# Kernel optimization log

Hardware: AMD Instinct MI355X
Metric: run time of the kernel (lower is better)

Reference implementation:

```python
import jax, jax.numpy as jnp
import numpy as np

K = 3; PAD = 1; CIN = 64; COUT = 64; B = 4; H = 128; W = 128


def setup_inputs() -> dict:
    key = jax.random.key(0)
    k1, k2, k3 = jax.random.split(key, 3)
    x = jax.random.normal(k1, (B, CIN, H, W), dtype=jnp.float32)
    # offset-predicting conv: [2*K*K, Cin, K, K]; small init -> sub-pixel offsets
    w_off = jax.random.normal(k2, (2 * K * K, CIN, K, K), dtype=jnp.float32) * 0.01
    b_off = jnp.zeros((2 * K * K,), dtype=jnp.float32)
    # deformable conv weight (bias=False): [Cout, Cin, K, K]
    w_def = jax.random.normal(k3, (COUT, CIN, K, K), dtype=jnp.float32) * 0.05
    return {"x": x, "w_off": w_off, "b_off": b_off, "w_def": w_def}


def _deform_conv(x, w_off, b_off, w_def):
    Bb, Cin, Hh, Ww = x.shape
    KK = K * K
    # 1) predict offsets with a regular 3x3 conv (stride 1, pad 1)
    off = jax.lax.conv_general_dilated(
        x, w_off, window_strides=(1, 1), padding=[(PAD, PAD), (PAD, PAD)],
        dimension_numbers=("NCHW", "OIHW", "NCHW"))
    off = off + b_off[None, :, None, None]          # [B, 2*KK, H, W]
    off = off.reshape(Bb, KK, 2, Hh, Ww)            # torchvision layout: (dy, dx) per tap
    dy, dx = off[:, :, 0], off[:, :, 1]             # [B, KK, H, W]

    # 2) sampling coordinates: p = p0 + p_k + offset
    ky = (jnp.arange(KK) // K).astype(x.dtype)
    kx = (jnp.arange(KK) % K).astype(x.dtype)
    hh = jnp.arange(Hh, dtype=x.dtype)
    ww = jnp.arange(Ww, dtype=x.dtype)
    py = hh[None, None, :, None] - PAD + ky[None, :, None, None] + dy   # [B,KK,H,W]
    px = ww[None, None, None, :] - PAD + kx[None, :, None, None] + dx

    # 3) bilinear sampling with zero padding outside the image
    y0f = jnp.floor(py); x0f = jnp.floor(px)
    fy = py - y0f; fx = px - x0f
    y0 = y0f.astype(jnp.int32); x0 = x0f.astype(jnp.int32)
    x_flat = x.reshape(Bb, Cin, Hh * Ww)

    def gather(yi, xi):
        valid = (yi >= 0) & (yi < Hh) & (xi >= 0) & (xi < Ww)
        idx = jnp.clip(yi, 0, Hh - 1) * Ww + jnp.clip(xi, 0, Ww - 1)     # [B,KK,H,W]
        g = jax.vmap(lambda xf, ix: xf[:, ix.reshape(-1)])(x_flat, idx)  # [B,Cin,KK*H*W]
        return g.reshape(Bb, Cin, KK, Hh, Ww) * valid[:, None].astype(x.dtype)

    sampled = (gather(y0, x0)         * ((1 - fy) * (1 - fx))[:, None]
             + gather(y0, x0 + 1)     * ((1 - fy) * fx)[:, None]
             + gather(y0 + 1, x0)     * (fy * (1 - fx))[:, None]
             + gather(y0 + 1, x0 + 1) * (fy * fx)[:, None])               # [B,Cin,KK,H,W]

    # 4) convolution accumulation over (Cin, kernel taps)
    return jnp.einsum('bckhw,ock->bohw', sampled, w_def.reshape(COUT, Cin, KK))


def reference(x, w_off, b_off, w_def):
    return _deform_conv(x, w_off, b_off, w_def)
```

## Files before the change

kernel.cpp:

```cpp
#include <hip/hip_runtime.h>
#include <hip/hip_fp16.h>

#define Bn   4
#define CINc 64
#define COUTc 64
#define Hn   128
#define Wn   128
#define HW   (Hn * Wn)
#define KKc  9
#define NOFF 18

typedef short bf16x8 __attribute__((ext_vector_type(8)));
typedef float f32x4  __attribute__((ext_vector_type(4)));
typedef float f32x2  __attribute__((ext_vector_type(2)));

__device__ inline unsigned short f2bf(float f) {
    unsigned int u = __float_as_uint(f);
    return (unsigned short)((u + 0x7fffu + ((u >> 16) & 1u)) >> 16);
}

__device__ inline void dma16(const void* g, void* l) {
#if __has_builtin(__builtin_amdgcn_global_load_lds)
    __builtin_amdgcn_global_load_lds(
        (__attribute__((address_space(1))) void*)(g),
        (__attribute__((address_space(3))) void*)(l), 16, 0, 0);
#else
    *(uint4*)l = *(const uint4*)g;
#endif
}

__global__ __launch_bounds__(256) void prep_all(
        const float* __restrict__ x, unsigned short* __restrict__ xt,
        const float* __restrict__ w_off, const float* __restrict__ w_def,
        unsigned short* __restrict__ wkb_sw, unsigned short* __restrict__ wob_sw) {
    int gb = blockIdx.x;
    int t  = threadIdx.x;
    if (gb < 1024) {
        __shared__ float s[64][65];
        int half = gb & 1;
        int h    = (gb >> 1) & 127;
        int b    = gb >> 8;
        int w0   = half * 64;

        const float* xb = x + (size_t)b * CINc * HW + (size_t)h * Wn + w0;
        int c0 = t >> 4, wq = (t & 15) * 4;
        #pragma unroll
        for (int i = 0; i < 4; ++i) {
            int c = c0 + i * 16;
            float4 v = *(const float4*)(xb + (size_t)c * HW + wq);
            s[c][wq]     = v.x;
            s[c][wq + 1] = v.y;
            s[c][wq + 2] = v.z;
            s[c][wq + 3] = v.w;
        }
        __syncthreads();

        int cpair = t & 31, pxg = t >> 5;
        unsigned* xtp = (unsigned*)xt;
        #pragma unroll
        for (int i = 0; i < 8; ++i) {
            int px = pxg * 8 + i;
            float v0 = s[cpair * 2][px], v1 = s[cpair * 2 + 1][px];
            unsigned d = (unsigned)f2bf(v0) | ((unsigned)f2bf(v1) << 16);
            xtp[(((size_t)(b * Hn + h) * Wn) + w0 + px) * 32 + cpair] = d;
        }
        return;
    }
    int idx = (gb - 1024) * 256 + t;
    if (idx < 36864) {
        int j = idx & 7, l = (idx >> 3) & 63, s = idx >> 9;
        int k = s >> 3, kc = (s >> 2) & 1, ot = s & 3;
        int l15 = l & 15, quad = l >> 4;
        int o = ot * 16 + l15, c = kc * 32 + quad * 8 + j;
        wkb_sw[idx] = f2bf(w_def[((size_t)o * 64 + c) * 9 + k]);
    }
    int i2 = idx - 36864;
    if (i2 >= 0 && i2 < 18432) {
        int j = i2 & 7, l = (i2 >> 3) & 63, s = i2 >> 9;
        int tt = s >> 2, kc = (s >> 1) & 1, mt = s & 1;
        int l15 = l & 15, quad = l >> 4;
        int m = mt * 16 + l15, c = kc * 32 + quad * 8 + j;
        unsigned short v = 0;
        if (m < NOFF) v = f2bf(w_off[((size_t)m * 64 + c) * 9 + tt]);
        wob_sw[i2] = v;
    }
}


#define BFBUILD(C, kc, BF, W0, W1, W2, W3)                                   \
    do {                                                                     \
        const unsigned* t0 = (const unsigned*)&(C)[(kc) * 4 + 0];            \
        const unsigned* t1 = (const unsigned*)&(C)[(kc) * 4 + 1];            \
        const unsigned* b0 = (const unsigned*)&(C)[(kc) * 4 + 2];            \
        const unsigned* b1 = (const unsigned*)&(C)[(kc) * 4 + 3];            \
        _Pragma("unroll")                                                    \
        for (int jd = 0; jd < 4; ++jd) {                                     \
            f32x2 t0p = {__uint_as_float(t0[jd] << 16),                      \
                         __uint_as_float(t0[jd] & 0xFFFF0000u)};             \
            f32x2 t1p = {__uint_as_float(t1[jd] << 16),                      \
                         __uint_as_float(t1[jd] & 0xFFFF0000u)};             \
            f32x2 b0p = {__uint_as_float(b0[jd] << 16),                      \
                         __uint_as_float(b0[jd] & 0xFFFF0000u)};             \
            f32x2 b1p = {__uint_as_float(b1[jd] << 16),                      \
                         __uint_as_float(b1[jd] & 0xFFFF0000u)};             \
            f32x2 vv = t0p * (W0) + t1p * (W1) + b0p * (W2) + b1p * (W3);    \
            unsigned pk;                                                     \
            asm("v_cvt_pk_bf16_f32 %0, %1, %2"                               \
                : "=v"(pk) : "v"(vv.x), "v"(vv.y));                          \
            (BF).u[jd] = pk;                                                 \
        }                                                                    \
    } while (0)

#define TAP(k)                                                               \
    do {                                                                     \
        const uint4* C = R[(k) & 1];                                         \
        union { unsigned u; __half2 hv; } c01, c23;                          \
        c01.u = pw01[(k)]; c23.u = pw23[(k)];                                \
        float W0 = __low2float(c01.hv), W1 = __high2float(c01.hv);           \
        float W2 = __low2float(c23.hv), W3 = __high2float(c23.hv);           \
        union { bf16x8 v; unsigned u[4]; } bfa, bfb;                         \
        BFBUILD(C, 0, bfa, W0, W1, W2, W3);                                  \
        BFBUILD(C, 1, bfb, W0, W1, W2, W3);                                  \
        _Pragma("unroll")                                                    \
        for (int ot = 0; ot < 4; ++ot) {                                     \
            bf16x8 af0 = s_wv[(((k) * 2 + 0) * 4 + ot) * 64 + lane];         \
            acc[ot] = __builtin_amdgcn_mfma_f32_16x16x32_bf16(               \
                af0, bfa.v, acc[ot], 0, 0, 0);                               \
            bf16x8 af1 = s_wv[(((k) * 2 + 1) * 4 + ot) * 64 + lane];         \
            acc[ot] = __builtin_amdgcn_mfma_f32_16x16x32_bf16(               \
                af1, bfb.v, acc[ot], 0, 0, 0);                               \
        }                                                                    \
    } while (0)

#define FETCH_G(kk, st)                                              \
    do {                                                             \
        unsigned ad_ = ad[kk];                                       \
        unsigned xc_ = ad_ >> 16;                                    \
        unsigned at_ = (((ad_ & 255u) << 7) + xc_) << 6;             \
        unsigned ab_ = ((((ad_ >> 8) & 255u) << 7) + xc_) << 6;      \
        R[st][0] = *(const uint4*)(xtb + at_ + co0);                 \
        R[st][1] = *(const uint4*)(xtb + at_ + 64 + co0);            \
        R[st][2] = *(const uint4*)(xtb + ab_ + co0);                 \
        R[st][3] = *(const uint4*)(xtb + ab_ + 64 + co0);            \
        R[st][4] = *(const uint4*)(xtb + at_ + co1);                 \
        R[st][5] = *(const uint4*)(xtb + at_ + 64 + co1);            \
        R[st][6] = *(const uint4*)(xtb + ab_ + co1);                 \
        R[st][7] = *(const uint4*)(xtb + ab_ + 64 + co1);            \
    } while (0)

#define FETCH_L(kk, st)                                              \
    do {                                                             \
        unsigned ad_ = ad[kk];                                       \
        int xc_ = (int)(ad_ >> 16);                                  \
        int r0_ = (int)(ad_ & 255u) - h + 2;                         \
        int r1_ = (int)((ad_ >> 8) & 255u) - h + 2;                  \
        int b00 = (r0_ * 128 + xc_) * 128;                           \
        int b10 = (r1_ * 128 + xc_) * 128;                           \
        int j0  = (quad ^ (xc_ & 7)) << 4;                           \
        int j1  = (quad ^ ((xc_ + 1) & 7)) << 4;                     \
        int j0b = ((4 + quad) ^ (xc_ & 7)) << 4;                     \
        int j1b = ((4 + quad) ^ ((xc_ + 1) & 7)) << 4;               \
        R[st][0] = *(const uint4*)(s_mem + b00 + j0);                \
        R[st][1] = *(const uint4*)(s_mem + b00 + 128 + j1);          \
        R[st][2] = *(const uint4*)(s_mem + b10 + j0);                \
        R[st][3] = *(const uint4*)(s_mem + b10 + 128 + j1);          \
        R[st][4] = *(const uint4*)(s_mem + b00 + j0b);               \
        R[st][5] = *(const uint4*)(s_mem + b00 + 128 + j1b);         \
        R[st][6] = *(const uint4*)(s_mem + b10 + j0b);               \
        R[st][7] = *(const uint4*)(s_mem + b10 + 128 + j1b);         \
    } while (0)

__global__ __launch_bounds__(512, 2) void fused_deform_v20(
        const unsigned short* __restrict__ xt,
        const unsigned short* __restrict__ wob_sw,
        const unsigned short* __restrict__ wkb_sw,
        const float* __restrict__ b_off, float* __restrict__ out) {
    extern __shared__ char s_mem[];
    bf16x8* s_wv = (bf16x8*)(s_mem + 81920);

    int gid  = blockIdx.x;
    int xcd  = gid & 7;
    int j    = gid >> 3;
    int hh   = j & 15;
    int b    = j >> 4;
    int h    = xcd * 16 + hh;
    int tid  = threadIdx.x;
    int lane = tid & 63;
    int wave = __builtin_amdgcn_readfirstlane(tid >> 6);
    int l15  = lane & 15;
    int quad = lane >> 4;
    int p    = wave * 16 + l15;

    const unsigned short* xtb = xt + (size_t)b * HW * 64;

    int xl = lane >> 3;
    int sl = lane & 7;
    #pragma unroll
    for (int i = 0; i < 10; ++i) {
        int slot = i * 8 + wave;
        int r  = slot >> 4;
        int g  = slot & 15;
        int y  = min(max(h - 2 + r, 0), Hn - 1);
        int xx = g * 8 + xl;
        int jj = sl ^ (xx & 7);
        dma16(xtb + ((size_t)y * Wn + xx) * 64 + jj * 8,
              s_mem + (size_t)r * 16384 + (size_t)g * 1024);
    }
    #pragma unroll
    for (int i = 0; i < 5; ++i) {
        int seg = i * 8 + wave;
        if (seg < 36)
            dma16((const uint4*)wob_sw + seg * 64 + lane,
                  s_mem + 81920 + (size_t)seg * 1024);
    }
    __syncthreads();

    f32x4 oa0 = (f32x4){0.f, 0.f, 0.f, 0.f};
    f32x4 oa1 = (f32x4){0.f, 0.f, 0.f, 0.f};
    #pragma unroll
    for (int t9 = 0; t9 < 9; ++t9) {
        int ty = t9 / 3, tx = t9 % 3;
        int y  = h - 1 + ty;
        int xg = p - 1 + tx;
        bool v = (y >= 0) && (y < Hn) && (xg >= 0) && (xg < Wn);
        unsigned m = v ? 0xFFFFFFFFu : 0u;
        int yc = min(max(y, 0), Hn - 1);
        int xc = min(max(xg, 0), Wn - 1);
        int r  = yc - h + 2;
        int base = (r * 128 + xc) * 128;
        uint4 L0 = *(const uint4*)(s_mem + base + ((quad ^ (xc & 7)) << 4));
        uint4 L1 = *(const uint4*)(s_mem + base + (((4 + quad) ^ (xc & 7)) << 4));
        #pragma unroll
        for (int kc = 0; kc < 2; ++kc) {
            union { bf16x8 v; uint4 u; } bf;
            bf.u = kc ? L1 : L0;
            bf.u.x &= m; bf.u.y &= m; bf.u.z &= m; bf.u.w &= m;
            bf16x8 a0 = s_wv[((t9 * 2 + kc) * 2 + 0) * 64 + lane];
            bf16x8 a1 = s_wv[((t9 * 2 + kc) * 2 + 1) * 64 + lane];
            oa0 = __builtin_amdgcn_mfma_f32_16x16x32_bf16(a0, bf.v, oa0, 0, 0, 0);
            oa1 = __builtin_amdgcn_mfma_f32_16x16x32_bf16(a1, bf.v, oa1, 0, 0, 0);
        }
    }

    unsigned my_ad[3]  = {0, 0, 0};
    unsigned my_w01[3] = {0, 0, 0};
    unsigned my_w23[3] = {0, 0, 0};
    auto phase1 = [&](int k, float dy, float dx, int slot) {
        float py  = (float)(h - 1 + k / 3) + dy;
        float pxf = (float)(p - 1 + k % 3) + dx;
        float y0f = floorf(py), x0f = floorf(pxf);
        float fy = py - y0f, fx = pxf - x0f;
        int y0 = (int)y0f, x0 = (int)x0f;
        bool vy0 = (y0 >= 0) & (y0 < Hn);
        bool vy1 = (y0 + 1 >= 0) & (y0 + 1 < Hn);
        bool vx0 = (x0 >= 0) & (x0 < Wn);
        bool vx1 = (x0 + 1 >= 0) & (x0 + 1 < Wn);
        float wy0 = vy0 ? 1.f - fy : 0.f;
        float wy1 = vy1 ? fy : 0.f;
        float wx0 = vx0 ? 1.f - fx : 0.f;
        float wx1 = vx1 ? fx : 0.f;
        int xc = min(max(x0, 0), Wn - 2);
        bool sel0 = (min(max(x0, 0), Wn - 1) != xc);
        bool sel1 = ((min(max(x0 + 1, 0), Wn - 1) - xc) == 1);
        float Wa = (sel0 ? 0.f : wx0) + (sel1 ? 0.f : wx1);
        float Wb = (sel0 ? wx0 : 0.f) + (sel1 ? wx1 : 0.f);
        int yc0 = min(max(y0, 0), Hn - 1), yc1 = min(max(y0 + 1, 0), Hn - 1);
        union { __half2 hv; unsigned u; } c01, c23;
        c01.hv = __floats2half2_rn(wy0 * Wa, wy0 * Wb);
        c23.hv = __floats2half2_rn(wy1 * Wa, wy1 * Wb);
        my_ad[slot]  = (unsigned)yc0 | ((unsigned)yc1 << 8) | ((unsigned)xc << 16);
        my_w01[slot] = c01.u;
        my_w23[slot] = c23.u;
    };
    int kb = quad * 2;
    phase1(kb,     oa0[0] + b_off[4 * quad],     oa0[1] + b_off[4 * quad + 1], 0);
    phase1(kb + 1, oa0[2] + b_off[4 * quad + 2], oa0[3] + b_off[4 * quad + 3], 1);
    if (quad == 0)
        phase1(8, oa1[0] + b_off[16], oa1[1] + b_off[17], 2);
    __syncthreads();

    #pragma unroll
    for (int i = 0; i < 9; ++i) {
        int seg = i * 8 + wave;
        dma16((const uint4*)wkb_sw + (size_t)seg * 64 + lane,
              s_mem + 81920 + (size_t)seg * 1024);
    }

    unsigned ad[KKc], pw01[KKc], pw23[KKc];
    #pragma unroll
    for (int k = 0; k < KKc; ++k) {
        int src  = (k < 8) ? ((k >> 1) * 16 + l15) : l15;
        int slot = (k < 8) ? (k & 1) : 2;
        ad[k]   = (unsigned)__shfl((int)my_ad[slot],  src, 64);
        pw01[k] = (unsigned)__shfl((int)my_w01[slot], src, 64);
        pw23[k] = (unsigned)__shfl((int)my_w23[slot], src, 64);
    }
    __syncthreads();

    bool oow = false;
    #pragma unroll
    for (int k = 0; k < KKc; ++k) {
        int r0 = (int)(ad[k] & 255u) - h + 2;
        int r1 = (int)((ad[k] >> 8) & 255u) - h + 2;
        oow |= ((unsigned)r0 > 4u) | ((unsigned)r1 > 4u);
    }
    bool use_global = __any(oow);

    f32x4 acc[4];
    #pragma unroll
    for (int ot = 0; ot < 4; ++ot) acc[ot] = (f32x4){0.f, 0.f, 0.f, 0.f};

    uint4 R[2][8];
    int co0 = quad * 8, co1 = 32 + quad * 8;

    if (__builtin_expect(use_global, 0)) {
        FETCH_G(0, 0);
        FETCH_G(1, 1); TAP(0);
        FETCH_G(2, 0); TAP(1);
        FETCH_G(3, 1); TAP(2);
        FETCH_G(4, 0); TAP(3);
        FETCH_G(5, 1); TAP(4);
        FETCH_G(6, 0); TAP(5);
        FETCH_G(7, 1); TAP(6);
        FETCH_G(8, 0); TAP(7);
        TAP(8);
    } else {
        FETCH_L(0, 0);
        FETCH_L(1, 1); TAP(0);
        FETCH_L(2, 0); TAP(1);
        FETCH_L(3, 1); TAP(2);
        FETCH_L(4, 0); TAP(3);
        FETCH_L(5, 1); TAP(4);
        FETCH_L(6, 0); TAP(5);
        FETCH_L(7, 1); TAP(6);
        FETCH_L(8, 0); TAP(7);
        TAP(8);
    }

    #pragma unroll
    for (int ot = 0; ot < 4; ++ot)
        #pragma unroll
        for (int rr = 0; rr < 4; ++rr) {
            int o = ot * 16 + quad * 4 + rr;
            out[(((size_t)b * COUTc + o) * Hn + h) * Wn + p] = acc[ot][rr];
        }
}

extern "C" void kernel_launch(void* const* d_in, const int* in_sizes, int n_in,
                              void* d_out, int out_size, void* d_ws, size_t ws_size,
                              hipStream_t stream) {
    const float* x     = (const float*)d_in[0];
    const float* w_off = (const float*)d_in[1];
    const float* b_off = (const float*)d_in[2];
    const float* w_def = (const float*)d_in[3];
    float* out = (float*)d_out;

    char* ws = (char*)d_ws;
    unsigned short* xt = (unsigned short*)ws;
    ws += (size_t)Bn * HW * CINc * sizeof(unsigned short);
    unsigned short* wkb_sw = (unsigned short*)ws;
    ws += 36864 * sizeof(unsigned short);
    unsigned short* wob_sw = (unsigned short*)ws;

    static bool attr_set = false;
    if (!attr_set) {
        (void)hipFuncSetAttribute((const void*)fused_deform_v20,
                                  hipFuncAttributeMaxDynamicSharedMemorySize,
                                  155648);
        attr_set = true;
    }

    prep_all<<<1024 + 216, 256, 0, stream>>>(x, xt, w_off, w_def, wkb_sw, wob_sw);
    fused_deform_v20<<<Bn * Hn, 512, 155648, stream>>>(xt, wob_sw, wkb_sw, b_off, out);
}
```

Baseline: 97.12 us.

## Switch operands from bf16 to fp16 and use packed fdot2 bilinear interpolation

Stores x and both weight sets as fp16 instead of bf16, and switches the MFMAs to the f16 variant. This lets the bilinear blend use v_perm plus fdot2 on packed halves in place of unpacking to fp32, doing four FMAs and packing. The aim is to cut VALU work in the gather-and-interpolate inner loop. fp16 has a narrower range than bf16, which is fine for these normal inputs and small weights, but the four-corner weighting now runs at half precision with an fp32 accumulate.

```diff
diff --git a/kernel.cpp b/kernel.cpp
--- a/kernel.cpp
+++ b/kernel.cpp
@@ -11,12 +11,12 @@
 #define NOFF 18
 
 typedef short bf16x8 __attribute__((ext_vector_type(8)));
+typedef _Float16 hf16x8 __attribute__((ext_vector_type(8)));
+typedef _Float16 hf16x2 __attribute__((ext_vector_type(2)));
 typedef float f32x4  __attribute__((ext_vector_type(4)));
-typedef float f32x2  __attribute__((ext_vector_type(2)));
-
-__device__ inline unsigned short f2bf(float f) {
-    unsigned int u = __float_as_uint(f);
-    return (unsigned short)((u + 0x7fffu + ((u >> 16) & 1u)) >> 16);
+
+__device__ inline unsigned short f2h(float f) {
+    return __half_as_ushort(__float2half(f));
 }
 
 __device__ inline void dma16(const void* g, void* l) {
@@ -61,7 +61,7 @@
         for (int i = 0; i < 8; ++i) {
             int px = pxg * 8 + i;
             float v0 = s[cpair * 2][px], v1 = s[cpair * 2 + 1][px];
-            unsigned d = (unsigned)f2bf(v0) | ((unsigned)f2bf(v1) << 16);
+            unsigned d = (unsigned)f2h(v0) | ((unsigned)f2h(v1) << 16);
             xtp[(((size_t)(b * Hn + h) * Wn) + w0 + px) * 32 + cpair] = d;
         }
         return;
@@ -72,7 +72,7 @@
         int k = s >> 3, kc = (s >> 2) & 1, ot = s & 3;
         int l15 = l & 15, quad = l >> 4;
         int o = ot * 16 + l15, c = kc * 32 + quad * 8 + j;
-        wkb_sw[idx] = f2bf(w_def[((size_t)o * 64 + c) * 9 + k]);
+        wkb_sw[idx] = f2h(w_def[((size_t)o * 64 + c) * 9 + k]);
     }
     int i2 = idx - 36864;
     if (i2 >= 0 && i2 < 18432) {
@@ -81,13 +81,15 @@
         int l15 = l & 15, quad = l >> 4;
         int m = mt * 16 + l15, c = kc * 32 + quad * 8 + j;
         unsigned short v = 0;
-        if (m < NOFF) v = f2bf(w_off[((size_t)m * 64 + c) * 9 + tt]);
+        if (m < NOFF) v = f2h(w_off[((size_t)m * 64 + c) * 9 + tt]);
         wob_sw[i2] = v;
     }
 }
 
 
-#define BFBUILD(C, kc, BF, W0, W1, W2, W3)                                   \
+#define AS_H2(u) __builtin_bit_cast(hf16x2, (unsigned)(u))
+
+#define BFBUILD(C, kc, BF, W01H, W23H)                                       \
     do {                                                                     \
         const unsigned* t0 = (const unsigned*)&(C)[(kc) * 4 + 0];            \
         const unsigned* t1 = (const unsigned*)&(C)[(kc) * 4 + 1];            \
@@ -95,39 +97,36 @@
         const unsigned* b1 = (const unsigned*)&(C)[(kc) * 4 + 3];            \
         _Pragma("unroll")                                                    \
         for (int jd = 0; jd < 4; ++jd) {                                     \
-            f32x2 t0p = {__uint_as_float(t0[jd] << 16),                      \
-                         __uint_as_float(t0[jd] & 0xFFFF0000u)};             \
-            f32x2 t1p = {__uint_as_float(t1[jd] << 16),                      \
-                         __uint_as_float(t1[jd] & 0xFFFF0000u)};             \
-            f32x2 b0p = {__uint_as_float(b0[jd] << 16),                      \
-                         __uint_as_float(b0[jd] & 0xFFFF0000u)};             \
-            f32x2 b1p = {__uint_as_float(b1[jd] << 16),                      \
-                         __uint_as_float(b1[jd] & 0xFFFF0000u)};             \
-            f32x2 vv = t0p * (W0) + t1p * (W1) + b0p * (W2) + b1p * (W3);    \
-            unsigned pk;                                                     \
-            asm("v_cvt_pk_bf16_f32 %0, %1, %2"                               \
-                : "=v"(pk) : "v"(vv.x), "v"(vv.y));                          \
-            (BF).u[jd] = pk;                                                 \
+            unsigned plt = __builtin_amdgcn_perm(t1[jd], t0[jd], 0x05040100u);\
+            unsigned pht = __builtin_amdgcn_perm(t1[jd], t0[jd], 0x07060302u);\
+            unsigned plb = __builtin_amdgcn_perm(b1[jd], b0[jd], 0x05040100u);\
+            unsigned phb = __builtin_amdgcn_perm(b1[jd], b0[jd], 0x07060302u);\
+            float lo = __builtin_amdgcn_fdot2(AS_H2(plt), (W01H),            \
+                       __builtin_amdgcn_fdot2(AS_H2(plb), (W23H), 0.f, false),\
+                       false);                                               \
+            float hi = __builtin_amdgcn_fdot2(AS_H2(pht), (W01H),            \
+                       __builtin_amdgcn_fdot2(AS_H2(phb), (W23H), 0.f, false),\
+                       false);                                               \
+            (BF).u[jd] = __builtin_bit_cast(unsigned,                        \
+                             __builtin_amdgcn_cvt_pkrtz(lo, hi));            \
         }                                                                    \
     } while (0)
 
 #define TAP(k)                                                               \
     do {                                                                     \
         const uint4* C = R[(k) & 1];                                         \
-        union { unsigned u; __half2 hv; } c01, c23;                          \
-        c01.u = pw01[(k)]; c23.u = pw23[(k)];                                \
-        float W0 = __low2float(c01.hv), W1 = __high2float(c01.hv);           \
-        float W2 = __low2float(c23.hv), W3 = __high2float(c23.hv);           \
-        union { bf16x8 v; unsigned u[4]; } bfa, bfb;                         \
-        BFBUILD(C, 0, bfa, W0, W1, W2, W3);                                  \
-        BFBUILD(C, 1, bfb, W0, W1, W2, W3);                                  \
+        hf16x2 W01H = AS_H2(pw01[(k)]);                                      \
+        hf16x2 W23H = AS_H2(pw23[(k)]);                                      \
+        union { hf16x8 v; unsigned u[4]; } bfa, bfb;                         \
+        BFBUILD(C, 0, bfa, W01H, W23H);                                      \
+        BFBUILD(C, 1, bfb, W01H, W23H);                                      \
         _Pragma("unroll")                                                    \
         for (int ot = 0; ot < 4; ++ot) {                                     \
-            bf16x8 af0 = s_wv[(((k) * 2 + 0) * 4 + ot) * 64 + lane];         \
-            acc[ot] = __builtin_amdgcn_mfma_f32_16x16x32_bf16(               \
+            hf16x8 af0 = s_wvh[(((k) * 2 + 0) * 4 + ot) * 64 + lane];        \
+            acc[ot] = __builtin_amdgcn_mfma_f32_16x16x32_f16(                \
                 af0, bfa.v, acc[ot], 0, 0, 0);                               \
-            bf16x8 af1 = s_wv[(((k) * 2 + 1) * 4 + ot) * 64 + lane];         \
-            acc[ot] = __builtin_amdgcn_mfma_f32_16x16x32_bf16(               \
+            hf16x8 af1 = s_wvh[(((k) * 2 + 1) * 4 + ot) * 64 + lane];        \
+            acc[ot] = __builtin_amdgcn_mfma_f32_16x16x32_f16(                \
                 af1, bfb.v, acc[ot], 0, 0, 0);                               \
         }                                                                    \
     } while (0)
@@ -170,13 +169,13 @@
         R[st][7] = *(const uint4*)(s_mem + b10 + 128 + j1b);         \
     } while (0)
 
-__global__ __launch_bounds__(512, 2) void fused_deform_v20(
+__global__ __launch_bounds__(512, 2) void fused_deform_v21(
         const unsigned short* __restrict__ xt,
         const unsigned short* __restrict__ wob_sw,
         const unsigned short* __restrict__ wkb_sw,
         const float* __restrict__ b_off, float* __restrict__ out) {
     extern __shared__ char s_mem[];
-    bf16x8* s_wv = (bf16x8*)(s_mem + 81920);
+    const hf16x8* s_wvh = (const hf16x8*)(s_mem + 81920);
 
     int gid  = blockIdx.x;
     int xcd  = gid & 7;
@@ -232,13 +231,13 @@
         uint4 L1 = *(const uint4*)(s_mem + base + (((4 + quad) ^ (xc & 7)) << 4));
         #pragma unroll
         for (int kc = 0; kc < 2; ++kc) {
-            union { bf16x8 v; uint4 u; } bf;
+            union { hf16x8 v; uint4 u; } bf;
             bf.u = kc ? L1 : L0;
             bf.u.x &= m; bf.u.y &= m; bf.u.z &= m; bf.u.w &= m;
-            bf16x8 a0 = s_wv[((t9 * 2 + kc) * 2 + 0) * 64 + lane];
-            bf16x8 a1 = s_wv[((t9 * 2 + kc) * 2 + 1) * 64 + lane];
-            oa0 = __builtin_amdgcn_mfma_f32_16x16x32_bf16(a0, bf.v, oa0, 0, 0, 0);
-            oa1 = __builtin_amdgcn_mfma_f32_16x16x32_bf16(a1, bf.v, oa1, 0, 0, 0);
+            hf16x8 a0 = s_wvh[((t9 * 2 + kc) * 2 + 0) * 64 + lane];
+            hf16x8 a1 = s_wvh[((t9 * 2 + kc) * 2 + 1) * 64 + lane];
+            oa0 = __builtin_amdgcn_mfma_f32_16x16x32_f16(a0, bf.v, oa0, 0, 0, 0);
+            oa1 = __builtin_amdgcn_mfma_f32_16x16x32_f16(a1, bf.v, oa1, 0, 0, 0);
         }
     }
 
@@ -364,12 +363,12 @@
 
     static bool attr_set = false;
     if (!attr_set) {
-        (void)hipFuncSetAttribute((const void*)fused_deform_v20,
+        (void)hipFuncSetAttribute((const void*)fused_deform_v21,
                                   hipFuncAttributeMaxDynamicSharedMemorySize,
                                   155648);
         attr_set = true;
     }
 
     prep_all<<<1024 + 216, 256, 0, stream>>>(x, xt, w_off, w_def, wkb_sw, wob_sw);
-    fused_deform_v20<<<Bn * Hn, 512, 155648, stream>>>(xt, wob_sw, wkb_sw, b_off, out);
-}
+    fused_deform_v21<<<Bn * Hn, 512, 155648, stream>>>(xt, wob_sw, wkb_sw, b_off, out);
+}
```

Result: no change. 97.37 us (+0.3%).

## Pad LDS pixel groups and restructure NHWC bf16 transpose prep kernel

Applied to the files above, without the earlier changes.

The fused kernel's LDS input tile gets a padded layout: every group of 8 pixels takes 1040 bytes instead of 1024, shifting bank mappings to cut conflicts in the bilinear gather and offset-conv loads. Every address computation (DMA destinations, FETCH_L, offset conv base) is updated to match, and dynamic LDS grows slightly. The prep kernel now does 256-pixel strips per block with bf16 conversion before the LDS transpose and paired stores, using fewer, larger blocks. The larger LDS footprint could affect occupancy at 2 blocks per CU.

```diff
diff --git a/kernel.cpp b/kernel.cpp
--- a/kernel.cpp
+++ b/kernel.cpp
@@ -10,6 +10,10 @@
 #define KKc  9
 #define NOFF 18
 
+#define GRP  1040
+#define ROWB (16 * GRP)
+#define WREG (5 * ROWB)
+
 typedef short bf16x8 __attribute__((ext_vector_type(8)));
 typedef float f32x4  __attribute__((ext_vector_type(4)));
 typedef float f32x2  __attribute__((ext_vector_type(2)));
@@ -35,38 +39,44 @@
         unsigned short* __restrict__ wkb_sw, unsigned short* __restrict__ wob_sw) {
     int gb = blockIdx.x;
     int t  = threadIdx.x;
-    if (gb < 1024) {
-        __shared__ float s[64][65];
-        int half = gb & 1;
-        int h    = (gb >> 1) & 127;
-        int b    = gb >> 8;
-        int w0   = half * 64;
-
-        const float* xb = x + (size_t)b * CINc * HW + (size_t)h * Wn + w0;
-        int c0 = t >> 4, wq = (t & 15) * 4;
+    if (gb < 256) {
+        __shared__ unsigned short s16[64][264];
+        int b  = gb >> 6;
+        int hp = gb & 63;
+        int w64 = t & 15, cg = t >> 4;
+
+        const float* xb = x + (size_t)b * CINc * HW + (size_t)hp * 256;
         #pragma unroll
-        for (int i = 0; i < 4; ++i) {
-            int c = c0 + i * 16;
-            float4 v = *(const float4*)(xb + (size_t)c * HW + wq);
-            s[c][wq]     = v.x;
-            s[c][wq + 1] = v.y;
-            s[c][wq + 2] = v.z;
-            s[c][wq + 3] = v.w;
+        for (int cc = 0; cc < 4; ++cc) {
+            int c = cg * 4 + cc;
+            #pragma unroll
+            for (int j = 0; j < 4; ++j) {
+                int px = j * 64 + w64 * 4;
+                float4 v = *(const float4*)(xb + (size_t)c * HW + px);
+                s16[c][px]     = f2bf(v.x);
+                s16[c][px + 1] = f2bf(v.y);
+                s16[c][px + 2] = f2bf(v.z);
+                s16[c][px + 3] = f2bf(v.w);
+            }
         }
         __syncthreads();
 
         int cpair = t & 31, pxg = t >> 5;
         unsigned* xtp = (unsigned*)xt;
+        size_t gbase = (size_t)b * HW + (size_t)hp * 256;
         #pragma unroll
-        for (int i = 0; i < 8; ++i) {
-            int px = pxg * 8 + i;
-            float v0 = s[cpair * 2][px], v1 = s[cpair * 2 + 1][px];
-            unsigned d = (unsigned)f2bf(v0) | ((unsigned)f2bf(v1) << 16);
-            xtp[(((size_t)(b * Hn + h) * Wn) + w0 + px) * 32 + cpair] = d;
+        for (int i = 0; i < 16; ++i) {
+            int px = pxg * 32 + i * 2;
+            unsigned a  = *(const unsigned*)&s16[cpair * 2][px];
+            unsigned bl = *(const unsigned*)&s16[cpair * 2 + 1][px];
+            unsigned d0 = (a & 0xFFFFu) | (bl << 16);
+            unsigned d1 = (a >> 16) | (bl & 0xFFFF0000u);
+            xtp[(gbase + px) * 32 + cpair]     = d0;
+            xtp[(gbase + px + 1) * 32 + cpair] = d1;
         }
         return;
     }
-    int idx = (gb - 1024) * 256 + t;
+    int idx = (gb - 256) * 256 + t;
     if (idx < 36864) {
         int j = idx & 7, l = (idx >> 3) & 63, s = idx >> 9;
         int k = s >> 3, kc = (s >> 2) & 1, ot = s & 3;
@@ -151,32 +161,33 @@
 #define FETCH_L(kk, st)                                              \
     do {                                                             \
         unsigned ad_ = ad[kk];                                       \
-        int xc_ = (int)(ad_ >> 16);                                  \
-        int r0_ = (int)(ad_ & 255u) - h + 2;                         \
-        int r1_ = (int)((ad_ >> 8) & 255u) - h + 2;                  \
-        int b00 = (r0_ * 128 + xc_) * 128;                           \
-        int b10 = (r1_ * 128 + xc_) * 128;                           \
-        int j0  = (quad ^ (xc_ & 7)) << 4;                           \
-        int j1  = (quad ^ ((xc_ + 1) & 7)) << 4;                     \
-        int j0b = ((4 + quad) ^ (xc_ & 7)) << 4;                     \
-        int j1b = ((4 + quad) ^ ((xc_ + 1) & 7)) << 4;               \
-        R[st][0] = *(const uint4*)(s_mem + b00 + j0);                \
-        R[st][1] = *(const uint4*)(s_mem + b00 + 128 + j1);          \
-        R[st][2] = *(const uint4*)(s_mem + b10 + j0);                \
-        R[st][3] = *(const uint4*)(s_mem + b10 + 128 + j1);          \
-        R[st][4] = *(const uint4*)(s_mem + b00 + j0b);               \
-        R[st][5] = *(const uint4*)(s_mem + b00 + 128 + j1b);         \
-        R[st][6] = *(const uint4*)(s_mem + b10 + j0b);               \
-        R[st][7] = *(const uint4*)(s_mem + b10 + 128 + j1b);         \
+        int x0_ = (int)(ad_ >> 16);                                  \
+        int x1_ = x0_ + 1;                                           \
+        int rt_ = ((int)(ad_ & 255u) - h + 2) * ROWB;                \
+        int rb_ = ((int)((ad_ >> 8) & 255u) - h + 2) * ROWB;         \
+        int a0_ = (x0_ >> 3) * GRP + (x0_ & 7) * 128;                \
+        int a1_ = (x1_ >> 3) * GRP + (x1_ & 7) * 128;                \
+        int j0  = (quad ^ (x0_ & 7)) << 4;                           \
+        int j1  = (quad ^ (x1_ & 7)) << 4;                           \
+        int j0b = ((4 + quad) ^ (x0_ & 7)) << 4;                     \
+        int j1b = ((4 + quad) ^ (x1_ & 7)) << 4;                     \
+        R[st][0] = *(const uint4*)(s_mem + rt_ + a0_ + j0);          \
+        R[st][1] = *(const uint4*)(s_mem + rt_ + a1_ + j1);          \
+        R[st][2] = *(const uint4*)(s_mem + rb_ + a0_ + j0);          \
+        R[st][3] = *(const uint4*)(s_mem + rb_ + a1_ + j1);          \
+        R[st][4] = *(const uint4*)(s_mem + rt_ + a0_ + j0b);         \
+        R[st][5] = *(const uint4*)(s_mem + rt_ + a1_ + j1b);         \
+        R[st][6] = *(const uint4*)(s_mem + rb_ + a0_ + j0b);         \
+        R[st][7] = *(const uint4*)(s_mem + rb_ + a1_ + j1b);         \
     } while (0)
 
-__global__ __launch_bounds__(512, 2) void fused_deform_v20(
+__global__ __launch_bounds__(512, 2) void fused_deform_v22(
         const unsigned short* __restrict__ xt,
         const unsigned short* __restrict__ wob_sw,
         const unsigned short* __restrict__ wkb_sw,
         const float* __restrict__ b_off, float* __restrict__ out) {
     extern __shared__ char s_mem[];
-    bf16x8* s_wv = (bf16x8*)(s_mem + 81920);
+    const bf16x8* s_wv = (const bf16x8*)(s_mem + WREG);
 
     int gid  = blockIdx.x;
     int xcd  = gid & 7;
@@ -204,14 +215,14 @@
         int xx = g * 8 + xl;
         int jj = sl ^ (xx & 7);
         dma16(xtb + ((size_t)y * Wn + xx) * 64 + jj * 8,
-              s_mem + (size_t)r * 16384 + (size_t)g * 1024);
+              s_mem + (size_t)r * ROWB + (size_t)g * GRP);
     }
     #pragma unroll
     for (int i = 0; i < 5; ++i) {
         int seg = i * 8 + wave;
         if (seg < 36)
             dma16((const uint4*)wob_sw + seg * 64 + lane,
-                  s_mem + 81920 + (size_t)seg * 1024);
+                  s_mem + WREG + (size_t)seg * 1024);
     }
     __syncthreads();
 
@@ -227,7 +238,7 @@
         int yc = min(max(y, 0), Hn - 1);
         int xc = min(max(xg, 0), Wn - 1);
         int r  = yc - h + 2;
-        int base = (r * 128 + xc) * 128;
+        int base = r * ROWB + (xc >> 3) * GRP + (xc & 7) * 128;
         uint4 L0 = *(const uint4*)(s_mem + base + ((quad ^ (xc & 7)) << 4));
         uint4 L1 = *(const uint4*)(s_mem + base + (((4 + quad) ^ (xc & 7)) << 4));
         #pragma unroll
@@ -283,7 +294,7 @@
     for (int i = 0; i < 9; ++i) {
         int seg = i * 8 + wave;
         dma16((const uint4*)wkb_sw + (size_t)seg * 64 + lane,
-              s_mem + 81920 + (size_t)seg * 1024);
+              s_mem + WREG + (size_t)seg * 1024);
     }
 
     unsigned ad[KKc], pw01[KKc], pw23[KKc];
@@ -364,12 +375,12 @@
 
     static bool attr_set = false;
     if (!attr_set) {
-        (void)hipFuncSetAttribute((const void*)fused_deform_v20,
+        (void)hipFuncSetAttribute((const void*)fused_deform_v22,
                                   hipFuncAttributeMaxDynamicSharedMemorySize,
-                                  155648);
+                                  156928);
         attr_set = true;
     }
 
-    prep_all<<<1024 + 216, 256, 0, stream>>>(x, xt, w_off, w_def, wkb_sw, wob_sw);
-    fused_deform_v20<<<Bn * Hn, 512, 155648, stream>>>(xt, wob_sw, wkb_sw, b_off, out);
-}
+    prep_all<<<256 + 216, 256, 0, stream>>>(x, xt, w_off, w_def, wkb_sw, wob_sw);
+    fused_deform_v22<<<Bn * Hn, 512, 156928, stream>>>(xt, wob_sw, wkb_sw, b_off, out);
+}
```

Result: no change. 97.41 us (+0.3%).
